# Kernel optimization log

Hardware: AMD Instinct MI355X
Metric: run time of the kernel (lower is better)

## Reference

```python
import jax, jax.numpy as jnp
import numpy as np

B, C, D, O = 4, 4096, 1024, 1024
PROJ = 256
RANKS = [1, 2, 4, 8]
E = len(RANKS)
CLAMP_MAX = float(np.log(1.0 / 0.01))  # log(100)


def setup_inputs() -> dict:
    key = jax.random.key(0)
    ks = jax.random.split(key, 16)
    inp = {
        "x": jax.random.normal(ks[0], (B, C, D), dtype=jnp.float32),
        "W": jax.random.normal(ks[1], (O, D), dtype=jnp.float32) / np.sqrt(D),
        "Wp": jax.random.normal(ks[2], (PROJ, D), dtype=jnp.float32) / np.sqrt(D),
        "bp": jnp.zeros((PROJ,), dtype=jnp.float32),
        "sim": jax.random.normal(ks[3], (PROJ, E), dtype=jnp.float32) * 0.01,
        "temp": jnp.full((1,), np.log(1.0 / 0.5), dtype=jnp.float32),
    }
    for i, r in enumerate(RANKS):
        inp[f"Wd{i}"] = jax.random.normal(ks[4 + 2 * i], (r, D), dtype=jnp.float32) / r
        inp[f"Wu{i}"] = jax.random.normal(ks[5 + 2 * i], (O, r), dtype=jnp.float32) * 0.01
    return inp


def _l2norm(v, axis):
    return v / jnp.maximum(jnp.linalg.norm(v, axis=axis, keepdims=True), 1e-12)


def reference(x, W, Wp, bp, sim, temp, Wd0, Wu0, Wd1, Wu1, Wd2, Wu2, Wd3, Wu3):
    # base linear (bias=False)
    base = jnp.einsum("bcd,od->bco", x, W)

    # cosine top-k gate on flattened tokens
    xf = x.reshape(-1, x.shape[-1])                         # [N, D]
    proj = _l2norm(xf @ Wp.T + bp, axis=1)                  # [N, PROJ]
    simn = _l2norm(sim, axis=0)                             # [PROJ, E]
    scale = jnp.exp(jnp.minimum(temp, CLAMP_MAX))
    logits = (proj @ simn) * scale                          # [N, E]

    # eval mode: no noise. softmax then top-1 mask * prob
    lw = jax.nn.softmax(logits, axis=1)
    top1 = jnp.argmax(lw, axis=1)                           # [N]
    ret = jnp.where(jnp.arange(E)[None, :] == top1[:, None], lw, 0.0)
    ret = ret.reshape(x.shape[0], x.shape[1], E)            # [B, C, E]

    # dense per-expert LoRA (ranks differ, so small fixed loop)
    downs = (Wd0, Wd1, Wd2, Wd3)
    ups = (Wu0, Wu1, Wu2, Wu3)
    l = jnp.stack(
        [jnp.einsum("bcr,or->bco", jnp.einsum("bcd,rd->bcr", x, d), u)
         for d, u in zip(downs, ups)],
        axis=2,
    )                                                       # [B, C, E, O]
    res = jnp.sum(ret[..., None] * l, axis=2)               # [B, C, O]
    return base + res
```

## Files before the change

kernel.cpp:

```cpp
#include <hip/hip_runtime.h>

#define TOK 16384
#define DD 1024
#define OO 1024
#define KE 1152
#define NT 18
#define NB1 288
#define CLAMPV 4.605170185988091f

typedef __attribute__((ext_vector_type(8))) short short8;
typedef __attribute__((ext_vector_type(4))) float f32x4;

__device__ __forceinline__ unsigned short f2bf(float f) {
  unsigned int u = __float_as_uint(f);
  return (unsigned short)((u + 0x7FFFu + ((u >> 16) & 1u)) >> 16);
}

__device__ __forceinline__ void gload16(const unsigned short* g, unsigned short* l) {
  __builtin_amdgcn_global_load_lds(
      (const __attribute__((address_space(1))) void*)g,
      (__attribute__((address_space(3))) void*)l, 16, 0, 0);
}

__device__ __forceinline__ float down_val(int j, int d,
    const float* __restrict__ Wd0, const float* __restrict__ Wd1,
    const float* __restrict__ Wd2, const float* __restrict__ Wd3) {
  if (j == 0) return Wd0[d];
  if (j < 3) return Wd1[(j - 1) * DD + d];
  if (j < 7) return Wd2[(j - 3) * DD + d];
  if (j < 15) return Wd3[(j - 7) * DD + d];
  return 0.f;
}

__global__ __launch_bounds__(256) void prep3(
    const float* __restrict__ W, const float* __restrict__ Wp,
    const float* __restrict__ sim, const float* __restrict__ bp,
    const float* __restrict__ Wd0, const float* __restrict__ Wd1,
    const float* __restrict__ Wd2, const float* __restrict__ Wd3,
    const float* __restrict__ Wu0, const float* __restrict__ Wu1,
    const float* __restrict__ Wu2, const float* __restrict__ Wu3,
    unsigned short* __restrict__ Bx, unsigned short* __restrict__ B1,
    unsigned short* __restrict__ Ax, float* __restrict__ v4,
    float* __restrict__ c4) {
  __shared__ float simn_l[256][4];
  __shared__ float part[4][4];
  const int tid = threadIdx.x;
  if (blockIdx.x < 4) {
    float4 sv = *(const float4*)&sim[tid * 4];
    float v[4] = {sv.x * sv.x, sv.y * sv.y, sv.z * sv.z, sv.w * sv.w};
#pragma unroll
    for (int off = 1; off < 64; off <<= 1) {
#pragma unroll
      for (int e = 0; e < 4; ++e) v[e] += __shfl_xor(v[e], off, 64);
    }
    int wv = tid >> 6, ln = tid & 63;
    if (ln == 0) { part[wv][0] = v[0]; part[wv][1] = v[1]; part[wv][2] = v[2]; part[wv][3] = v[3]; }
    __syncthreads();
    float n0 = fmaxf(sqrtf(part[0][0] + part[1][0] + part[2][0] + part[3][0]), 1e-12f);
    float n1 = fmaxf(sqrtf(part[0][1] + part[1][1] + part[2][1] + part[3][1]), 1e-12f);
    float n2 = fmaxf(sqrtf(part[0][2] + part[1][2] + part[2][2] + part[3][2]), 1e-12f);
    float n3 = fmaxf(sqrtf(part[0][3] + part[1][3] + part[2][3] + part[3][3]), 1e-12f);
    simn_l[tid][0] = sv.x / n0; simn_l[tid][1] = sv.y / n1;
    simn_l[tid][2] = sv.z / n2; simn_l[tid][3] = sv.w / n3;
    __syncthreads();
    int d = blockIdx.x * 256 + tid;
    float a0 = 0.f, a1 = 0.f, a2 = 0.f, a3 = 0.f;
    for (int j = 0; j < 256; ++j) {
      float w = Wp[j * DD + d];
      a0 = __builtin_fmaf(w, simn_l[j][0], a0);
      a1 = __builtin_fmaf(w, simn_l[j][1], a1);
      a2 = __builtin_fmaf(w, simn_l[j][2], a2);
      a3 = __builtin_fmaf(w, simn_l[j][3], a3);
    }
    v4[d] = a0; v4[1024 + d] = a1; v4[2048 + d] = a2; v4[3072 + d] = a3;
    if (blockIdx.x == 0) {
      float bpv = bp[tid];
      float pc[4] = {simn_l[tid][0] * bpv, simn_l[tid][1] * bpv,
                     simn_l[tid][2] * bpv, simn_l[tid][3] * bpv};
#pragma unroll
      for (int off = 1; off < 64; off <<= 1) {
#pragma unroll
        for (int e = 0; e < 4; ++e) pc[e] += __shfl_xor(pc[e], off, 64);
      }
      __syncthreads();
      if (ln == 0) { part[wv][0] = pc[0]; part[wv][1] = pc[1]; part[wv][2] = pc[2]; part[wv][3] = pc[3]; }
      __syncthreads();
      if (tid == 0) {
#pragma unroll
        for (int e = 0; e < 4; ++e)
          c4[e] = part[0][e] + part[1][e] + part[2][e] + part[3][e];
      }
    }
  }
  const int nB1 = NB1 * DD;
  const int nWb = OO * KE;
  const int nXpad = TOK * 112;
  const int total = nB1 + nWb + nXpad;
  for (int i = blockIdx.x * 256 + tid; i < total; i += gridDim.x * 256) {
    if (i < nB1) {
      int r = i >> 10, c = i & 1023;
      float v = 0.f;
      if (r < 256) v = Wp[r * DD + c];
      else if (r < 271) v = down_val(r - 256, c, Wd0, Wd1, Wd2, Wd3);
      B1[i] = f2bf(v);
    } else if (i < nB1 + nWb) {
      int j = i - nB1;
      int o = j / KE, c = j - o * KE;
      float v = 0.f;
      if (c < 1024) v = W[o * DD + c];
      else if (c == 1024) v = Wu0[o];
      else if (c < 1027) v = Wu1[o * 2 + (c - 1025)];
      else if (c < 1031) v = Wu2[o * 4 + (c - 1027)];
      else if (c < 1039) v = Wu3[o * 8 + (c - 1031)];
      Bx[j] = f2bf(v);
    } else {
      int j = i - nB1 - nWb;
      int row = j / 112, c = j - row * 112;
      Ax[row * KE + 1040 + c] = 0;
    }
  }
}

__global__ __launch_bounds__(512, 1) void gemm2f(
    const float* __restrict__ x, const float* __restrict__ v4,
    unsigned short* __restrict__ Ax, const unsigned short* __restrict__ B1,
    const float* __restrict__ c4, const float* __restrict__ bp,
    const float* __restrict__ temp) {
  __shared__ __align__(16) unsigned short as1[2][64 * 32];
  __shared__ __align__(16) unsigned short bs1[2][NB1 * 32];
  __shared__ float ssq_s[2][64];
  __shared__ float xdown_s[64][16];
  __shared__ __align__(16) float dots_s[64][4];
  const int tid = threadIdx.x;
  const int lane = tid & 63, wv = tid >> 6;
  const int wm = wv >> 1, wn = wv & 1;
  const int r0 = blockIdx.x * 64;
  const int ro = lane & 15, ko = (lane >> 4) * 8;
  const int srow = lane >> 2, scol = (lane & 3) * 8;
  const int xr = tid >> 3;
  const int xc = (tid & 7) * 4;
  const float* xgp = &x[(r0 + xr) * DD + xc];
  unsigned short* axp = &Ax[(r0 + xr) * KE + xc];
  f32x4 acc[9] = {};
  float dotp[4] = {};

#define STB1(KT, BUF)                                                         \
  for (int c = wv; c < 18; c += 8)                                            \
    gload16(&B1[(c * 16 + srow) * DD + (KT) * 32 + scol], &bs1[BUF][c * 512]);

#define XSTG(KT, BUF) do {                                                    \
    float4 xv = *(const float4*)(xgp + (KT) * 32);                            \
    float4 va = *(const float4*)&v4[(KT) * 32 + xc];                          \
    float4 vb = *(const float4*)&v4[1024 + (KT) * 32 + xc];                   \
    float4 vc = *(const float4*)&v4[2048 + (KT) * 32 + xc];                   \
    float4 vd = *(const float4*)&v4[3072 + (KT) * 32 + xc];                   \
    dotp[0] = __builtin_fmaf(xv.x, va.x, __builtin_fmaf(xv.y, va.y,           \
              __builtin_fmaf(xv.z, va.z, __builtin_fmaf(xv.w, va.w, dotp[0])))); \
    dotp[1] = __builtin_fmaf(xv.x, vb.x, __builtin_fmaf(xv.y, vb.y,           \
              __builtin_fmaf(xv.z, vb.z, __builtin_fmaf(xv.w, vb.w, dotp[1])))); \
    dotp[2] = __builtin_fmaf(xv.x, vc.x, __builtin_fmaf(xv.y, vc.y,           \
              __builtin_fmaf(xv.z, vc.z, __builtin_fmaf(xv.w, vc.w, dotp[2])))); \
    dotp[3] = __builtin_fmaf(xv.x, vd.x, __builtin_fmaf(xv.y, vd.y,           \
              __builtin_fmaf(xv.z, vd.z, __builtin_fmaf(xv.w, vd.w, dotp[3])))); \
    union { unsigned short s[4]; uint2 q; } pk;                               \
    pk.s[0] = f2bf(xv.x); pk.s[1] = f2bf(xv.y);                               \
    pk.s[2] = f2bf(xv.z); pk.s[3] = f2bf(xv.w);                               \
    *reinterpret_cast<uint2*>(axp + (KT) * 32) = pk.q;                        \
    *reinterpret_cast<uint2*>(&as1[BUF][xr * 32 + xc]) = pk.q;                \
  } while (0)

  XSTG(0, 0);
  STB1(0, 0)
  __syncthreads();
  int cur = 0;
  for (int kt = 0; kt < 32; ++kt) {
    if (kt < 31) {
      XSTG(kt + 1, cur ^ 1);
      STB1(kt + 1, cur ^ 1)
    }
    const unsigned short* ap = &as1[cur][0];
    const unsigned short* bpp = &bs1[cur][0];
    short8 af = *reinterpret_cast<const short8*>(ap + (wm * 16 + ro) * 32 + ko);
#pragma unroll
    for (int n = 0; n < 9; ++n) {
      short8 bf = *reinterpret_cast<const short8*>(bpp + (wn * 144 + n * 16 + ro) * 32 + ko);
      acc[n] = __builtin_amdgcn_mfma_f32_16x16x32_bf16(af, bf, acc[n], 0, 0, 0);
    }
    if (kt < 31) {
      __syncthreads();
      cur ^= 1;
    }
  }

#pragma unroll
  for (int off = 1; off < 8; off <<= 1) {
#pragma unroll
    for (int e = 0; e < 4; ++e) dotp[e] += __shfl_xor(dotp[e], off, 64);
  }
  if ((lane & 7) == 0) {
    dots_s[xr][0] = dotp[0]; dots_s[xr][1] = dotp[1];
    dots_s[xr][2] = dotp[2]; dots_s[xr][3] = dotp[3];
  }

  float ssqp[4] = {};
#pragma unroll
  for (int n = 0; n < 9; ++n) {
    int col = wn * 144 + n * 16 + ro;
    if (col < 256) {
      float b = bp[col];
#pragma unroll
      for (int r = 0; r < 4; ++r) {
        float a = acc[n][r] + b;
        ssqp[r] = __builtin_fmaf(a, a, ssqp[r]);
      }
    }
  }
#pragma unroll
  for (int off = 1; off < 16; off <<= 1) {
#pragma unroll
    for (int r = 0; r < 4; ++r) ssqp[r] += __shfl_xor(ssqp[r], off, 64);
  }
  if (ro == 0) {
#pragma unroll
    for (int r = 0; r < 4; ++r)
      ssq_s[wn][wm * 16 + (lane >> 4) * 4 + r] = ssqp[r];
  }
  if (wn == 1 && ro < 15) {
#pragma unroll
    for (int r = 0; r < 4; ++r)
      xdown_s[wm * 16 + (lane >> 4) * 4 + r][ro] = acc[7][r];
  }
  __syncthreads();

  if (tid < 64) {
    const int row = tid, t = r0 + row;
    float ssqT = ssq_s[0][row] + ssq_s[1][row];
    float4 cc = *reinterpret_cast<const float4*>(c4);
    float scale = expf(fminf(temp[0], CLAMPV));
    float inv = scale / fmaxf(sqrtf(ssqT), 1e-12f);
    float l[4];
    l[0] = (dots_s[row][0] + cc.x) * inv; l[1] = (dots_s[row][1] + cc.y) * inv;
    l[2] = (dots_s[row][2] + cc.z) * inv; l[3] = (dots_s[row][3] + cc.w) * inv;
    int be = 0; float m = l[0];
    if (l[1] > m) { m = l[1]; be = 1; }
    if (l[2] > m) { m = l[2]; be = 2; }
    if (l[3] > m) { m = l[3]; be = 3; }
    float den = expf(l[0] - m) + expf(l[1] - m) + expf(l[2] - m) + expf(l[3] - m);
    float g = 1.0f / den;
    int off = (1 << be) - 1;
    int rr = 1 << be;
    union { unsigned short s[16]; uint4 v[2]; } o;
#pragma unroll
    for (int j = 0; j < 16; ++j) {
      float dv = xdown_s[row][j & 15];
      float v = (j >= off && j < off + rr) ? g * dv : 0.f;
      o.s[j] = f2bf(v);
    }
    uint4* dst = reinterpret_cast<uint4*>(&Ax[t * KE + 1024]);
    dst[0] = o.v[0];
    dst[1] = o.v[1];
  }
}

__global__ __launch_bounds__(512, 2) void main_gemm8(
    const unsigned short* __restrict__ A, const unsigned short* __restrict__ Bm,
    float* __restrict__ C) {
  __shared__ __align__(16) unsigned short lbuf[2][32768];
  const int tid = threadIdx.x;
  const int lane = tid & 63, wv = tid >> 6;
  const int wm = wv >> 2, wn = wv & 3;
  const int dd = blockIdx.x;
  const int tt = (dd & 7) * 32 + (dd >> 3);
  const int bx = tt & 3, by = tt >> 2;
  const int r0 = by * 256, c0 = bx * 256;
  const int ro = lane & 15, ko = (lane >> 4) * 8;
  const int rowb = ro * 128;
  const int swz = (ro & 7) << 4;
  const int lk0 = (ko * 2) ^ swz;
  const int lk1 = (64 + ko * 2) ^ swz;
  const int ll = (lane * 16) ^ ((lane >> 3) << 4);
  const int sro = ll >> 7;
  const int sk = (ll & 127) >> 1;
  f32x4 acc[8][4] = {};
  short8 Af[4][2], B0[2][2], B1r[2][2];

#define STG(MTX, GRB, HBU, BUF, U2)                                           \
  do {                                                                        \
    gload16(&MTX[((GRB) + (0 * 8 + wv) * 8 + sro) * KE + (U2) * 64 + sk],     \
            &lbuf[BUF][(HBU) + (0 * 8 + wv) * 512]);                          \
    gload16(&MTX[((GRB) + (1 * 8 + wv) * 8 + sro) * KE + (U2) * 64 + sk],     \
            &lbuf[BUF][(HBU) + (1 * 8 + wv) * 512]);                          \
  } while (0)

#define LDA(FI, QM, LK) (*reinterpret_cast<const short8*>(                    \
    (const char*)Ab + wm * 16384 + (QM) * 8192 + (FI) * 2048 + rowb + (LK)))
#define LDB(FN, QN, LK) (*reinterpret_cast<const short8*>(                    \
    (const char*)Bb + wn * 8192 + (QN) * 4096 + (FN) * 2048 + rowb + (LK)))

#define MMQ(QM, QN, BF)                                                       \
  do {                                                                        \
    _Pragma("unroll")                                                         \
    for (int fi = 0; fi < 4; ++fi) {                                          \
      _Pragma("unroll")                                                       \
      for (int fn = 0; fn < 2; ++fn) {                                        \
        acc[(QM)*4+fi][(QN)*2+fn] = __builtin_amdgcn_mfma_f32_16x16x32_bf16(  \
            Af[fi][0], BF[fn][0], acc[(QM)*4+fi][(QN)*2+fn], 0, 0, 0);        \
        acc[(QM)*4+fi][(QN)*2+fn] = __builtin_amdgcn_mfma_f32_16x16x32_bf16(  \
            Af[fi][1], BF[fn][1], acc[(QM)*4+fi][(QN)*2+fn], 0, 0, 0);        \
      }                                                                       \
    }                                                                         \
  } while (0)

  STG(Bm, c0,       16384, 0, 0);
  STG(A,  r0,       0,     0, 0);
  STG(Bm, c0 + 128, 24576, 0, 0);
  STG(A,  r0 + 128, 8192,  0, 0);
  STG(Bm, c0,       16384, 1, 1);
  STG(A,  r0,       0,     1, 1);
  asm volatile("s_waitcnt vmcnt(4)" ::: "memory");
  __builtin_amdgcn_s_barrier();

  for (int u = 0; u < NT; ++u) {
    const int db = u & 1;
    const unsigned short* Ab = &lbuf[db][0];
    const unsigned short* Bb = &lbuf[db][16384];
#pragma unroll
    for (int fi = 0; fi < 4; ++fi) { Af[fi][0] = LDA(fi, 0, lk0); Af[fi][1] = LDA(fi, 0, lk1); }
#pragma unroll
    for (int fn = 0; fn < 2; ++fn) { B0[fn][0] = LDB(fn, 0, lk0); B0[fn][1] = LDB(fn, 0, lk1); }
    if (u + 1 < NT) STG(Bm, c0 + 128, 24576, (u + 1) & 1, u + 1);
    __builtin_amdgcn_s_barrier();
    __builtin_amdgcn_s_setprio(1);
    MMQ(0, 0, B0);
    __builtin_amdgcn_s_setprio(0);
    __builtin_amdgcn_s_barrier();
#pragma unroll
    for (int fn = 0; fn < 2; ++fn) { B1r[fn][0] = LDB(fn, 1, lk0); B1r[fn][1] = LDB(fn, 1, lk1); }
    if (u + 1 < NT) STG(A, r0 + 128, 8192, (u + 1) & 1, u + 1);
    __builtin_amdgcn_s_barrier();
    __builtin_amdgcn_s_setprio(1);
    MMQ(0, 1, B1r);
    __builtin_amdgcn_s_setprio(0);
    __builtin_amdgcn_s_barrier();
#pragma unroll
    for (int fi = 0; fi < 4; ++fi) { Af[fi][0] = LDA(fi, 1, lk0); Af[fi][1] = LDA(fi, 1, lk1); }
    if (u + 2 < NT) STG(Bm, c0, 16384, db, u + 2);
    __builtin_amdgcn_s_barrier();
    __builtin_amdgcn_s_setprio(1);
    MMQ(1, 1, B1r);
    __builtin_amdgcn_s_setprio(0);
    __builtin_amdgcn_s_barrier();
    if (u + 2 < NT) STG(A, r0, 0, db, u + 2);
    __builtin_amdgcn_s_barrier();
    __builtin_amdgcn_s_setprio(1);
    MMQ(1, 0, B0);
    __builtin_amdgcn_s_setprio(0);
    if (u + 2 < NT) {
      asm volatile("s_waitcnt vmcnt(4)" ::: "memory");
    } else if (u == NT - 2) {
      asm volatile("s_waitcnt vmcnt(0)" ::: "memory");
    }
    __builtin_amdgcn_s_barrier();
  }

#pragma unroll
  for (int m = 0; m < 8; ++m) {
    int rr = r0 + wm * 128 + m * 16 + (lane >> 4) * 4;
#pragma unroll
    for (int n = 0; n < 4; ++n) {
      int cc = c0 + wn * 64 + n * 16 + ro;
#pragma unroll
      for (int v = 0; v < 4; ++v)
        C[(rr + v) * OO + cc] = acc[m][n][v];
    }
  }
#undef STG
#undef LDA
#undef LDB
#undef MMQ
}

extern "C" void kernel_launch(void* const* d_in, const int* in_sizes, int n_in,
                              void* d_out, int out_size, void* d_ws, size_t ws_size,
                              hipStream_t stream) {
  const float* x    = (const float*)d_in[0];
  const float* W    = (const float*)d_in[1];
  const float* Wp   = (const float*)d_in[2];
  const float* bp   = (const float*)d_in[3];
  const float* sim  = (const float*)d_in[4];
  const float* temp = (const float*)d_in[5];
  const float* Wd0  = (const float*)d_in[6];
  const float* Wu0  = (const float*)d_in[7];
  const float* Wd1  = (const float*)d_in[8];
  const float* Wu1  = (const float*)d_in[9];
  const float* Wd2  = (const float*)d_in[10];
  const float* Wu2  = (const float*)d_in[11];
  const float* Wd3  = (const float*)d_in[12];
  const float* Wu3  = (const float*)d_in[13];
  float* out = (float*)d_out;
  char* ws = (char*)d_ws;
  unsigned short* Ax  = (unsigned short*)ws;
  unsigned short* Bx  = (unsigned short*)(ws + 37748736);
  unsigned short* B1  = (unsigned short*)(ws + 40108032);
  float* v4           = (float*)(ws + 40697856);
  float* c4           = (float*)(ws + 40714240);

  prep3<<<1024, 256, 0, stream>>>(W, Wp, sim, bp, Wd0, Wd1, Wd2, Wd3,
                                  Wu0, Wu1, Wu2, Wu3, Bx, B1, Ax, v4, c4);
  gemm2f<<<256, 512, 0, stream>>>(x, v4, Ax, B1, c4, bp, temp);
  main_gemm8<<<256, 512, 0, stream>>>(Ax, Bx, out);
}
```

Measured before the change: 108.1 us.

## Trim augmented GEMM K padding and software-pipeline x loads in gate GEMM

The padded K width of the augmented main GEMM drops from 1152 to 1088 (17 k-tiles instead of 18), so the 1039 real columns are padded less and the main GEMM does fewer MFMAs and loads less. The gate GEMM (gemm2f) now prefetches x and v4 registers two tiles ahead, with explicit vmcnt waits and raw s_barrier in place of __syncthreads, so global loads overlap the MFMA work. The hand-written waitcnt counts depend on exact instruction ordering and could race if the compiler schedules loads differently. Workspace offsets shift to match the smaller Ax and Bx buffers.

```diff
diff --git a/kernel.cpp b/kernel.cpp
--- a/kernel.cpp
+++ b/kernel.cpp
@@ -3,8 +3,8 @@
 #define TOK 16384
 #define DD 1024
 #define OO 1024
-#define KE 1152
-#define NT 18
+#define KE 1088
+#define NT 17
 #define NB1 288
 #define CLAMPV 4.605170185988091f
 
@@ -94,7 +94,7 @@
   }
   const int nB1 = NB1 * DD;
   const int nWb = OO * KE;
-  const int nXpad = TOK * 112;
+  const int nXpad = TOK * 48;
   const int total = nB1 + nWb + nXpad;
   for (int i = blockIdx.x * 256 + tid; i < total; i += gridDim.x * 256) {
     if (i < nB1) {
@@ -115,7 +115,7 @@
       Bx[j] = f2bf(v);
     } else {
       int j = i - nB1 - nWb;
-      int row = j / 112, c = j - row * 112;
+      int row = j / 48, c = j - row * 48;
       Ax[row * KE + 1040 + c] = 0;
     }
   }
@@ -143,17 +143,22 @@
   unsigned short* axp = &Ax[(r0 + xr) * KE + xc];
   f32x4 acc[9] = {};
   float dotp[4] = {};
+  float4 xv, va, vb, vc, vd;
+  float4 xn, na, nb, nc, nd;
 
 #define STB1(KT, BUF)                                                         \
   for (int c = wv; c < 18; c += 8)                                            \
     gload16(&B1[(c * 16 + srow) * DD + (KT) * 32 + scol], &bs1[BUF][c * 512]);
 
-#define XSTG(KT, BUF) do {                                                    \
-    float4 xv = *(const float4*)(xgp + (KT) * 32);                            \
-    float4 va = *(const float4*)&v4[(KT) * 32 + xc];                          \
-    float4 vb = *(const float4*)&v4[1024 + (KT) * 32 + xc];                   \
-    float4 vc = *(const float4*)&v4[2048 + (KT) * 32 + xc];                   \
-    float4 vd = *(const float4*)&v4[3072 + (KT) * 32 + xc];                   \
+#define LOADX(KT, X, VA, VB, VC, VD) do {                                     \
+    X  = *(const float4*)(xgp + (KT) * 32);                                   \
+    VA = *(const float4*)&v4[(KT) * 32 + xc];                                 \
+    VB = *(const float4*)&v4[1024 + (KT) * 32 + xc];                          \
+    VC = *(const float4*)&v4[2048 + (KT) * 32 + xc];                          \
+    VD = *(const float4*)&v4[3072 + (KT) * 32 + xc];                          \
+  } while (0)
+
+#define PROC(KT, BUF) do {                                                    \
     dotp[0] = __builtin_fmaf(xv.x, va.x, __builtin_fmaf(xv.y, va.y,           \
               __builtin_fmaf(xv.z, va.z, __builtin_fmaf(xv.w, va.w, dotp[0])))); \
     dotp[1] = __builtin_fmaf(xv.x, vb.x, __builtin_fmaf(xv.y, vb.y,           \
@@ -169,26 +174,44 @@
     *reinterpret_cast<uint2*>(&as1[BUF][xr * 32 + xc]) = pk.q;                \
   } while (0)
 
-  XSTG(0, 0);
+#define MM(BUF) do {                                                          \
+    const unsigned short* ap = &as1[BUF][0];                                  \
+    const unsigned short* bpp = &bs1[BUF][0];                                 \
+    short8 af = *reinterpret_cast<const short8*>(ap + (wm * 16 + ro) * 32 + ko); \
+    _Pragma("unroll")                                                         \
+    for (int n = 0; n < 9; ++n) {                                             \
+      short8 bf = *reinterpret_cast<const short8*>(                           \
+          bpp + (wn * 144 + n * 16 + ro) * 32 + ko);                          \
+      acc[n] = __builtin_amdgcn_mfma_f32_16x16x32_bf16(af, bf, acc[n], 0, 0, 0); \
+    }                                                                         \
+  } while (0)
+
+  LOADX(0, xv, va, vb, vc, vd);
   STB1(0, 0)
-  __syncthreads();
-  int cur = 0;
-  for (int kt = 0; kt < 32; ++kt) {
-    if (kt < 31) {
-      XSTG(kt + 1, cur ^ 1);
-      STB1(kt + 1, cur ^ 1)
-    }
-    const unsigned short* ap = &as1[cur][0];
-    const unsigned short* bpp = &bs1[cur][0];
-    short8 af = *reinterpret_cast<const short8*>(ap + (wm * 16 + ro) * 32 + ko);
-#pragma unroll
-    for (int n = 0; n < 9; ++n) {
-      short8 bf = *reinterpret_cast<const short8*>(bpp + (wn * 144 + n * 16 + ro) * 32 + ko);
-      acc[n] = __builtin_amdgcn_mfma_f32_16x16x32_bf16(af, bf, acc[n], 0, 0, 0);
-    }
-    if (kt < 31) {
-      __syncthreads();
-      cur ^= 1;
+  __builtin_amdgcn_sched_barrier(0);
+  PROC(0, 0);
+  LOADX(1, xn, na, nb, nc, nd);
+  asm volatile("s_waitcnt vmcnt(6) lgkmcnt(0)" ::: "memory");
+  __builtin_amdgcn_s_barrier();
+  xv = xn; va = na; vb = nb; vc = nc; vd = nd;
+
+  for (int u = 0; u < 32; ++u) {
+    const int cb = u & 1;
+    if (u < 31) {
+      STB1(u + 1, cb ^ 1)
+      __builtin_amdgcn_sched_barrier(0);
+      PROC(u + 1, cb ^ 1);
+      if (u < 30) LOADX(u + 2, xn, na, nb, nc, nd);
+    }
+    MM(cb);
+    if (u < 31) {
+      if (u < 30) {
+        asm volatile("s_waitcnt vmcnt(6) lgkmcnt(0)" ::: "memory");
+      } else {
+        asm volatile("s_waitcnt vmcnt(1) lgkmcnt(0)" ::: "memory");
+      }
+      __builtin_amdgcn_s_barrier();
+      xv = xn; va = na; vb = nb; vc = nc; vd = nd;
     }
   }
 
@@ -260,6 +283,10 @@
     dst[0] = o.v[0];
     dst[1] = o.v[1];
   }
+#undef STB1
+#undef LOADX
+#undef PROC
+#undef MM
 }
 
 __global__ __launch_bounds__(512, 2) void main_gemm8(
@@ -400,10 +427,10 @@
   float* out = (float*)d_out;
   char* ws = (char*)d_ws;
   unsigned short* Ax  = (unsigned short*)ws;
-  unsigned short* Bx  = (unsigned short*)(ws + 37748736);
-  unsigned short* B1  = (unsigned short*)(ws + 40108032);
-  float* v4           = (float*)(ws + 40697856);
-  float* c4           = (float*)(ws + 40714240);
+  unsigned short* Bx  = (unsigned short*)(ws + 35651584);
+  unsigned short* B1  = (unsigned short*)(ws + 37879808);
+  float* v4           = (float*)(ws + 38469632);
+  float* c4           = (float*)(ws + 38486016);
 
   prep3<<<1024, 256, 0, stream>>>(W, Wp, sim, bp, Wd0, Wd1, Wd2, Wd3,
                                   Wu0, Wu1, Wu2, Wu3, Bx, B1, Ax, v4, c4);
```

After: 107.0 us. No clear change (-1.1%).
